# Kernel tuning notes

Measured on AMD Instinct MI355X. Metric: run time of the kernel, lower is better.

## Reference

```python
import jax, jax.numpy as jnp
import numpy as np

B, S, D = 64, 512, 1024   # batch, max_phon_seq_len, d_model
V = 64                    # phonological vocabulary size
T = 131072                # total ragged tokens (avg 4 per (batch, position) slot)


def setup_inputs() -> dict:
    key = jax.random.key(0)
    k1, k2, k3, k4 = jax.random.split(key, 4)
    tokens = jax.random.randint(k1, (T,), 0, V)                      # flat token indices
    segment_ids = jnp.sort(jax.random.randint(k2, (T,), 0, B * S))   # sorted segment id per token
    phon_embedding = jax.random.normal(k3, (V, D), dtype=jnp.float32)
    phon_pos_embedding = jax.random.normal(k4, (S, D), dtype=jnp.float32)
    return {
        "tokens": tokens,
        "segment_ids": segment_ids,
        "phon_embedding": phon_embedding,
        "phon_pos_embedding": phon_pos_embedding,
    }


def reference(tokens, segment_ids, phon_embedding, phon_pos_embedding):
    # Fused ragged segment-mean embedding (EmbeddingBag 'mean' semantics):
    # for each (batch, position) segment, mean of embeddings of its tokens.
    gathered = phon_embedding[tokens]                                   # [T, D]
    sums = jax.ops.segment_sum(gathered, segment_ids, num_segments=B * S)          # [B*S, D]
    counts = jax.ops.segment_sum(jnp.ones((T,), dtype=gathered.dtype),
                                 segment_ids, num_segments=B * S)       # [B*S]
    means = sums / jnp.maximum(counts, 1.0)[:, None]                    # empty slots stay zero
    # add positional embedding, as in embed_phon_tokens
    out = means.reshape(B, S, D) + phon_pos_embedding[None, :, :]       # [B, S, D]
    return out
```

## Files before the change

### kernel.cpp

```cpp
#include <hip/hip_runtime.h>
#include <hip/hip_bf16.h>

#define BB 64
#define SS 512
#define DD 1024
#define NSEG (BB * SS)

typedef float floatx4 __attribute__((ext_vector_type(4)));

__global__ __launch_bounds__(256) void fill_bounds_kernel(
    const int* __restrict__ seg_ids,
    int* __restrict__ seg_start,
    int T)
{
    int t = blockIdx.x * blockDim.x + threadIdx.x;
    if (t >= T) return;
    int cur  = seg_ids[t];
    int prev = (t == 0) ? -1 : seg_ids[t - 1];
    for (int s = prev + 1; s <= cur; ++s) seg_start[s] = t;
    if (t == T - 1) {
        for (int s = cur + 1; s <= NSEG; ++s) seg_start[s] = T;
    }
}

__global__ __launch_bounds__(256) void seg_mean_embed_kernel(
    const int* __restrict__ tokens,
    const int* __restrict__ seg_start,
    const float* __restrict__ emb,
    const float* __restrict__ pos,
    float* __restrict__ out)
{
    const int seg = blockIdx.x;
    const int lo = seg_start[seg];
    const int hi = seg_start[seg + 1];

    const int d = threadIdx.x * 4;

    floatx4 acc = (floatx4)(0.f);
    for (int t = lo; t < hi; ++t) {
        const int tok = tokens[t];
        const floatx4 v = *reinterpret_cast<const floatx4*>(emb + (size_t)tok * DD + d);
        acc += v;
    }

    const int cnt = hi - lo;
    const float inv = (cnt > 0) ? (1.0f / (float)cnt) : 0.0f;

    const int s = seg & (SS - 1);
    const floatx4 p = *reinterpret_cast<const floatx4*>(pos + (size_t)s * DD + d);

    floatx4 o = acc * inv + p;

    *reinterpret_cast<floatx4*>(out + (size_t)seg * DD + d) = o;
}

__device__ __forceinline__ int lower_bound_dev(const int* __restrict__ a, int n, int key) {
    int lo = 0, hi = n;
    while (lo < hi) {
        int mid = (lo + hi) >> 1;
        if (a[mid] < key) lo = mid + 1; else hi = mid;
    }
    return lo;
}

__global__ __launch_bounds__(256) void seg_mean_embed_bsearch_kernel(
    const int* __restrict__ tokens,
    const int* __restrict__ seg_ids,
    const float* __restrict__ emb,
    const float* __restrict__ pos,
    float* __restrict__ out,
    int T)
{
    const int seg = blockIdx.x;
    const int lo = lower_bound_dev(seg_ids, T, seg);
    const int hi = lower_bound_dev(seg_ids, T, seg + 1);
    const int d = threadIdx.x * 4;

    floatx4 acc = (floatx4)(0.f);
    for (int t = lo; t < hi; ++t) {
        const int tok = tokens[t];
        const floatx4 v = *reinterpret_cast<const floatx4*>(emb + (size_t)tok * DD + d);
        acc += v;
    }
    const int cnt = hi - lo;
    const float inv = (cnt > 0) ? (1.0f / (float)cnt) : 0.0f;
    const int s = seg & (SS - 1);
    const floatx4 p = *reinterpret_cast<const floatx4*>(pos + (size_t)s * DD + d);
    floatx4 o = acc * inv + p;
    *reinterpret_cast<floatx4*>(out + (size_t)seg * DD + d) = o;
}

extern "C" void kernel_launch(void* const* d_in, const int* in_sizes, int n_in,
                              void* d_out, int out_size, void* d_ws, size_t ws_size,
                              hipStream_t stream) {
    const int*   tokens  = (const int*)d_in[0];
    const int*   seg_ids = (const int*)d_in[1];
    const float* emb     = (const float*)d_in[2];
    const float* pos     = (const float*)d_in[3];
    float*       out     = (float*)d_out;
    const int T = in_sizes[0];

    const size_t need = (size_t)(NSEG + 1) * sizeof(int);
    if (ws_size >= need) {
        int* seg_start = (int*)d_ws;
        fill_bounds_kernel<<<(T + 255) / 256, 256, 0, stream>>>(seg_ids, seg_start, T);
        seg_mean_embed_kernel<<<NSEG, 256, 0, stream>>>(tokens, seg_start, emb, pos, out);
    } else {
        seg_mean_embed_bsearch_kernel<<<NSEG, 256, 0, stream>>>(tokens, seg_ids, emb, pos, out, T);
    }
}
```

Measured before the change: 43.14 us.

## Stage embedding table halves in LDS as bf16 and batch segments per block

Replaces the one-block-per-segment kernel with blocks that each copy half of the 64x1024 embedding table into shared memory, converted to bf16. Each block then processes 128 segments, one wave per segment at a time, with 8 columns per lane. The aim is to cut repeated global/L2 gathers of embedding rows and the per-block launch overhead. In exchange, every block redundantly loads and converts 128KB of the table, and the 64KB of LDS per block limits occupancy. Storing the table in bf16 also adds rounding error to the means, which is a precision trade-off.

```diff
diff --git a/kernel.cpp b/kernel.cpp
--- a/kernel.cpp
+++ b/kernel.cpp
@@ -4,9 +4,25 @@
 #define BB 64
 #define SS 512
 #define DD 1024
+#define VV 64
 #define NSEG (BB * SS)
+#define HALF 512
+#define SEGS_PER_BLK 128
+#define THREADS 512
 
 typedef float floatx4 __attribute__((ext_vector_type(4)));
+
+__device__ __forceinline__ ushort f32_to_bf16_rne(float f) {
+    unsigned int b = __float_as_uint(f);
+    unsigned int r = b + 0x7fffu + ((b >> 16) & 1u);
+    return (ushort)(r >> 16);
+}
+__device__ __forceinline__ float bf16lo_to_f32(unsigned int u) {
+    return __uint_as_float(u << 16);
+}
+__device__ __forceinline__ float bf16hi_to_f32(unsigned int u) {
+    return __uint_as_float(u & 0xffff0000u);
+}
 
 __global__ __launch_bounds__(256) void fill_bounds_kernel(
     const int* __restrict__ seg_ids,
@@ -23,35 +39,74 @@
     }
 }
 
-__global__ __launch_bounds__(256) void seg_mean_embed_kernel(
+__global__ __launch_bounds__(THREADS, 4) void seg_mean_lds_kernel(
     const int* __restrict__ tokens,
     const int* __restrict__ seg_start,
     const float* __restrict__ emb,
     const float* __restrict__ pos,
     float* __restrict__ out)
 {
-    const int seg = blockIdx.x;
-    const int lo = seg_start[seg];
-    const int hi = seg_start[seg + 1];
+    __shared__ ushort s_emb[VV * HALF];
 
-    const int d = threadIdx.x * 4;
+    const int bid     = blockIdx.x;
+    const int half    = bid & 1;
+    const int segbase = (bid >> 1) * SEGS_PER_BLK;
+    const int tid     = threadIdx.x;
 
-    floatx4 acc = (floatx4)(0.f);
-    for (int t = lo; t < hi; ++t) {
-        const int tok = tokens[t];
-        const floatx4 v = *reinterpret_cast<const floatx4*>(emb + (size_t)tok * DD + d);
-        acc += v;
+    const float* src = emb + half * HALF;
+    #pragma unroll
+    for (int k = 0; k < (VV * HALF) / (THREADS * 4); ++k) {
+        const int flat = k * THREADS * 4 + tid * 4;
+        const int row  = flat >> 9;
+        const int col  = flat & (HALF - 1);
+        const floatx4 v = *reinterpret_cast<const floatx4*>(src + (size_t)row * DD + col);
+        ushort4 u;
+        u.x = f32_to_bf16_rne(v.x);
+        u.y = f32_to_bf16_rne(v.y);
+        u.z = f32_to_bf16_rne(v.z);
+        u.w = f32_to_bf16_rne(v.w);
+        *reinterpret_cast<ushort4*>(&s_emb[flat]) = u;
     }
+    __syncthreads();
 
-    const int cnt = hi - lo;
-    const float inv = (cnt > 0) ? (1.0f / (float)cnt) : 0.0f;
+    const int wave    = tid >> 6;
+    const int lane    = tid & 63;
+    const int colbase = lane * 8;
 
-    const int s = seg & (SS - 1);
-    const floatx4 p = *reinterpret_cast<const floatx4*>(pos + (size_t)s * DD + d);
+    #pragma unroll 1
+    for (int i = 0; i < SEGS_PER_BLK / 8; ++i) {
+        const int seg = segbase + i * 8 + wave;
+        const int lo  = seg_start[seg];
+        const int hi  = seg_start[seg + 1];
 
-    floatx4 o = acc * inv + p;
+        float acc[8] = {0.f, 0.f, 0.f, 0.f, 0.f, 0.f, 0.f, 0.f};
+        for (int t = lo; t < hi; ++t) {
+            const int tok = tokens[t];
+            const uint4 u = *reinterpret_cast<const uint4*>(&s_emb[tok * HALF + colbase]);
+            acc[0] += bf16lo_to_f32(u.x); acc[1] += bf16hi_to_f32(u.x);
+            acc[2] += bf16lo_to_f32(u.y); acc[3] += bf16hi_to_f32(u.y);
+            acc[4] += bf16lo_to_f32(u.z); acc[5] += bf16hi_to_f32(u.z);
+            acc[6] += bf16lo_to_f32(u.w); acc[7] += bf16hi_to_f32(u.w);
+        }
 
-    *reinterpret_cast<floatx4*>(out + (size_t)seg * DD + d) = o;
+        const int cnt = hi - lo;
+        const float inv = (cnt > 0) ? (1.0f / (float)cnt) : 0.0f;
+
+        const int s = seg & (SS - 1);
+        const float* pp = pos + (size_t)s * DD + half * HALF + colbase;
+        const floatx4 p0 = *reinterpret_cast<const floatx4*>(pp);
+        const floatx4 p1 = *reinterpret_cast<const floatx4*>(pp + 4);
+
+        floatx4 o0, o1;
+        o0.x = acc[0] * inv + p0.x;  o0.y = acc[1] * inv + p0.y;
+        o0.z = acc[2] * inv + p0.z;  o0.w = acc[3] * inv + p0.w;
+        o1.x = acc[4] * inv + p1.x;  o1.y = acc[5] * inv + p1.y;
+        o1.z = acc[6] * inv + p1.z;  o1.w = acc[7] * inv + p1.w;
+
+        float* op = out + (size_t)seg * DD + half * HALF + colbase;
+        *reinterpret_cast<floatx4*>(op)     = o0;
+        *reinterpret_cast<floatx4*>(op + 4) = o1;
+    }
 }
 
 __device__ __forceinline__ int lower_bound_dev(const int* __restrict__ a, int n, int key) {
@@ -104,7 +159,8 @@
     if (ws_size >= need) {
         int* seg_start = (int*)d_ws;
         fill_bounds_kernel<<<(T + 255) / 256, 256, 0, stream>>>(seg_ids, seg_start, T);
-        seg_mean_embed_kernel<<<NSEG, 256, 0, stream>>>(tokens, seg_start, emb, pos, out);
+        const int grid = (NSEG / SEGS_PER_BLK) * 2;
+        seg_mean_lds_kernel<<<grid, THREADS, 0, stream>>>(tokens, seg_start, emb, pos, out);
     } else {
         seg_mean_embed_bsearch_kernel<<<NSEG, 256, 0, stream>>>(tokens, seg_ids, emb, pos, out, T);
     }
```

After: 50.93 us. 1.18x slower.

## Group eight segments per block, stage tokens in LDS, gather bf16 table

Applied to the files above, without the earlier changes.

Converts the fp32 embedding table to a bf16 copy in workspace with a small pre-kernel. The main kernel processes eight segments per block, staging their token indices in shared memory, then accumulates bf16 rows in fp32. Output is written with nontemporal stores. The aim is to cut block launch overhead and gather traffic and to avoid polluting the cache with output. In exchange it adds a kernel launch and reduces embedding precision.

```diff
diff --git a/kernel.cpp b/kernel.cpp
--- a/kernel.cpp
+++ b/kernel.cpp
@@ -4,9 +4,24 @@
 #define BB 64
 #define SS 512
 #define DD 1024
+#define VV 64
 #define NSEG (BB * SS)
+#define G_SEGS 8
+#define CAP 2048
 
 typedef float floatx4 __attribute__((ext_vector_type(4)));
+
+__device__ __forceinline__ ushort f32_to_bf16_rne(float f) {
+    unsigned int b = __float_as_uint(f);
+    unsigned int r = b + 0x7fffu + ((b >> 16) & 1u);
+    return (ushort)(r >> 16);
+}
+__device__ __forceinline__ float bf16lo_to_f32(unsigned int u) {
+    return __uint_as_float(u << 16);
+}
+__device__ __forceinline__ float bf16hi_to_f32(unsigned int u) {
+    return __uint_as_float(u & 0xffff0000u);
+}
 
 __global__ __launch_bounds__(256) void fill_bounds_kernel(
     const int* __restrict__ seg_ids,
@@ -23,35 +38,74 @@
     }
 }
 
-__global__ __launch_bounds__(256) void seg_mean_embed_kernel(
+__global__ __launch_bounds__(256) void conv_emb_kernel(
+    const float* __restrict__ emb,
+    ushort* __restrict__ tbl)
+{
+    const int i = (blockIdx.x * 256 + threadIdx.x) * 4;
+    const floatx4 v = *reinterpret_cast<const floatx4*>(emb + i);
+    ushort4 u;
+    u.x = f32_to_bf16_rne(v.x);
+    u.y = f32_to_bf16_rne(v.y);
+    u.z = f32_to_bf16_rne(v.z);
+    u.w = f32_to_bf16_rne(v.w);
+    *reinterpret_cast<ushort4*>(tbl + i) = u;
+}
+
+__global__ __launch_bounds__(256) void seg_mean_g8_kernel(
     const int* __restrict__ tokens,
     const int* __restrict__ seg_start,
-    const float* __restrict__ emb,
+    const ushort* __restrict__ tbl,
     const float* __restrict__ pos,
     float* __restrict__ out)
 {
-    const int seg = blockIdx.x;
-    const int lo = seg_start[seg];
-    const int hi = seg_start[seg + 1];
+    __shared__ int s_bnd[G_SEGS + 1];
+    __shared__ int s_tok[CAP];
 
-    const int d = threadIdx.x * 4;
+    const int g0  = blockIdx.x * G_SEGS;
+    const int tid = threadIdx.x;
 
-    floatx4 acc = (floatx4)(0.f);
-    for (int t = lo; t < hi; ++t) {
-        const int tok = tokens[t];
-        const floatx4 v = *reinterpret_cast<const floatx4*>(emb + (size_t)tok * DD + d);
-        acc += v;
+    if (tid <= G_SEGS) s_bnd[tid] = seg_start[g0 + tid];
+    __syncthreads();
+
+    const int lo0   = s_bnd[0];
+    const int total = s_bnd[G_SEGS] - lo0;
+    const int n_lds = (total < CAP) ? total : CAP;
+    for (int j = tid; j < n_lds; j += 256) s_tok[j] = tokens[lo0 + j];
+    __syncthreads();
+
+    const int d = tid * 4;
+
+    #pragma unroll 1
+    for (int s = 0; s < G_SEGS; ++s) {
+        const int seg = g0 + s;
+        const int lo  = s_bnd[s];
+        const int hi  = s_bnd[s + 1];
+
+        float a0 = 0.f, a1 = 0.f, a2 = 0.f, a3 = 0.f;
+        for (int t = lo; t < hi; ++t) {
+            const int idx = t - lo0;
+            const int tok = (idx < CAP) ? s_tok[idx] : tokens[t];
+            const uint2 u = *reinterpret_cast<const uint2*>(tbl + tok * DD + d);
+            a0 += bf16lo_to_f32(u.x); a1 += bf16hi_to_f32(u.x);
+            a2 += bf16lo_to_f32(u.y); a3 += bf16hi_to_f32(u.y);
+        }
+
+        const int cnt = hi - lo;
+        const float inv = (cnt > 0) ? (1.0f / (float)cnt) : 0.0f;
+
+        const floatx4 p = *reinterpret_cast<const floatx4*>(
+            pos + (size_t)(seg & (SS - 1)) * DD + d);
+
+        floatx4 o;
+        o.x = a0 * inv + p.x;
+        o.y = a1 * inv + p.y;
+        o.z = a2 * inv + p.z;
+        o.w = a3 * inv + p.w;
+
+        __builtin_nontemporal_store(o, reinterpret_cast<floatx4*>(
+            out + (size_t)seg * DD + d));
     }
-
-    const int cnt = hi - lo;
-    const float inv = (cnt > 0) ? (1.0f / (float)cnt) : 0.0f;
-
-    const int s = seg & (SS - 1);
-    const floatx4 p = *reinterpret_cast<const floatx4*>(pos + (size_t)s * DD + d);
-
-    floatx4 o = acc * inv + p;
-
-    *reinterpret_cast<floatx4*>(out + (size_t)seg * DD + d) = o;
 }
 
 __device__ __forceinline__ int lower_bound_dev(const int* __restrict__ a, int n, int key) {
@@ -100,11 +154,14 @@
     float*       out     = (float*)d_out;
     const int T = in_sizes[0];
 
-    const size_t need = (size_t)(NSEG + 1) * sizeof(int);
+    const size_t tbl_bytes = (size_t)VV * DD * sizeof(ushort);
+    const size_t need = tbl_bytes + (size_t)(NSEG + 1) * sizeof(int);
     if (ws_size >= need) {
-        int* seg_start = (int*)d_ws;
+        ushort* tbl       = (ushort*)d_ws;
+        int*    seg_start = (int*)((char*)d_ws + tbl_bytes);
         fill_bounds_kernel<<<(T + 255) / 256, 256, 0, stream>>>(seg_ids, seg_start, T);
-        seg_mean_embed_kernel<<<NSEG, 256, 0, stream>>>(tokens, seg_start, emb, pos, out);
+        conv_emb_kernel<<<(VV * DD) / (256 * 4), 256, 0, stream>>>(emb, tbl);
+        seg_mean_g8_kernel<<<NSEG / G_SEGS, 256, 0, stream>>>(tokens, seg_start, tbl, pos, out);
     } else {
         seg_mean_embed_bsearch_kernel<<<NSEG, 256, 0, stream>>>(tokens, seg_ids, emb, pos, out, T);
     }
```

Result: slower. 47.03 us (+9.0%).

## Recast segment-mean embedding as token-count histogram times bf16 embedding GEMM

Applied to the files above, without the earlier changes.

Builds a per-segment token histogram over the 64-word vocabulary, swizzles the embedding table into bf16 MFMA operand layout, and computes segment sums as a matrix multiply with MFMA instructions, fusing the mean scaling and positional add into the epilogue with nontemporal stores. This replaces per-token gathers of embedding rows with dense matrix math. In exchange it adds two extra kernel launches, a histogram buffer round-trip through memory, and reduces embedding precision to bf16.

```diff
diff --git a/kernel.cpp b/kernel.cpp
--- a/kernel.cpp
+++ b/kernel.cpp
@@ -4,9 +4,17 @@
 #define BB 64
 #define SS 512
 #define DD 1024
+#define VV 64
 #define NSEG (BB * SS)
 
-typedef float floatx4 __attribute__((ext_vector_type(4)));
+typedef float f32x4 __attribute__((ext_vector_type(4)));
+typedef short bf16x8 __attribute__((ext_vector_type(8)));
+
+__device__ __forceinline__ ushort f32_to_bf16_rne(float f) {
+    unsigned int b = __float_as_uint(f);
+    unsigned int r = b + 0x7fffu + ((b >> 16) & 1u);
+    return (ushort)(r >> 16);
+}
 
 __global__ __launch_bounds__(256) void fill_bounds_kernel(
     const int* __restrict__ seg_ids,
@@ -23,35 +31,129 @@
     }
 }
 
-__global__ __launch_bounds__(256) void seg_mean_embed_kernel(
+__global__ __launch_bounds__(256) void build_h_kernel(
     const int* __restrict__ tokens,
     const int* __restrict__ seg_start,
+    float* __restrict__ H)
+{
+    __shared__ float h[256 * VV];
+    const int tid  = threadIdx.x;
+    const int seg0 = blockIdx.x * 256;
+    for (int i = tid; i < 256 * VV; i += 256) h[i] = 0.f;
+    __syncthreads();
+    const int seg = seg0 + tid;
+    const int lo = seg_start[seg];
+    const int hi = seg_start[seg + 1];
+    for (int t = lo; t < hi; ++t) h[tid * VV + tokens[t]] += 1.f;
+    __syncthreads();
+    const f32x4* src = (const f32x4*)h;
+    f32x4* dst = (f32x4*)(H + (size_t)seg0 * VV);
+    for (int i = tid; i < 256 * VV / 4; i += 256) dst[i] = src[i];
+}
+
+__global__ __launch_bounds__(256) void swz_emb_kernel(
     const float* __restrict__ emb,
+    ushort* __restrict__ A)
+{
+    const int g    = blockIdx.x * 256 + threadIdx.x;
+    const int lane = g & 63;
+    const int tile = g >> 6;
+    const int ks   = tile & 1;
+    const int mt   = tile >> 1;
+    const int dim  = mt * 16 + (lane & 15);
+    const int v0   = ks * 32 + (lane >> 4) * 8;
+    bf16x8 w;
+    #pragma unroll
+    for (int j = 0; j < 8; ++j)
+        w[j] = (short)f32_to_bf16_rne(emb[(size_t)(v0 + j) * DD + dim]);
+    *reinterpret_cast<bf16x8*>(A + (size_t)g * 8) = w;
+}
+
+#define MW 64
+#define NW 32
+__global__ __launch_bounds__(256) void gemm_kernel(
+    const ushort* __restrict__ A,
+    const float* __restrict__ H,
+    const int* __restrict__ seg_start,
     const float* __restrict__ pos,
     float* __restrict__ out)
 {
-    const int seg = blockIdx.x;
-    const int lo = seg_start[seg];
-    const int hi = seg_start[seg + 1];
-
-    const int d = threadIdx.x * 4;
-
-    floatx4 acc = (floatx4)(0.f);
-    for (int t = lo; t < hi; ++t) {
-        const int tok = tokens[t];
-        const floatx4 v = *reinterpret_cast<const floatx4*>(emb + (size_t)tok * DD + d);
-        acc += v;
-    }
-
-    const int cnt = hi - lo;
-    const float inv = (cnt > 0) ? (1.0f / (float)cnt) : 0.0f;
-
-    const int s = seg & (SS - 1);
-    const floatx4 p = *reinterpret_cast<const floatx4*>(pos + (size_t)s * DD + d);
-
-    floatx4 o = acc * inv + p;
-
-    *reinterpret_cast<floatx4*>(out + (size_t)seg * DD + d) = o;
+    const int warp = threadIdx.x >> 6;
+    const int lane = threadIdx.x & 63;
+    const int mgrp = blockIdx.x & 15;
+    const int ngrp = blockIdx.x >> 4;
+    const int m_base = mgrp * MW;
+    const int n_base = ngrp * (NW * 4) + warp * NW;
+
+    const int mt0 = m_base >> 4;
+    bf16x8 a[4][2];
+    #pragma unroll
+    for (int mi = 0; mi < 4; ++mi)
+        #pragma unroll
+        for (int ks = 0; ks < 2; ++ks)
+            a[mi][ks] = *reinterpret_cast<const bf16x8*>(
+                A + ((size_t)((mt0 + mi) * 2 + ks) * 64 + lane) * 8);
+
+    bf16x8 b[2][2];
+    #pragma unroll
+    for (int ni = 0; ni < 2; ++ni) {
+        const int seg = n_base + ni * 16 + (lane & 15);
+        const float* hrow = H + (size_t)seg * VV + (lane >> 4) * 8;
+        #pragma unroll
+        for (int ks = 0; ks < 2; ++ks) {
+            const f32x4 h0 = *reinterpret_cast<const f32x4*>(hrow + ks * 32);
+            const f32x4 h1 = *reinterpret_cast<const f32x4*>(hrow + ks * 32 + 4);
+            bf16x8 w;
+            w[0] = (short)(__float_as_uint(h0[0]) >> 16);
+            w[1] = (short)(__float_as_uint(h0[1]) >> 16);
+            w[2] = (short)(__float_as_uint(h0[2]) >> 16);
+            w[3] = (short)(__float_as_uint(h0[3]) >> 16);
+            w[4] = (short)(__float_as_uint(h1[0]) >> 16);
+            w[5] = (short)(__float_as_uint(h1[1]) >> 16);
+            w[6] = (short)(__float_as_uint(h1[2]) >> 16);
+            w[7] = (short)(__float_as_uint(h1[3]) >> 16);
+            b[ni][ks] = w;
+        }
+    }
+
+    f32x4 acc[4][2];
+    #pragma unroll
+    for (int mi = 0; mi < 4; ++mi)
+        #pragma unroll
+        for (int ni = 0; ni < 2; ++ni)
+            acc[mi][ni] = (f32x4)(0.f);
+
+    #pragma unroll
+    for (int ks = 0; ks < 2; ++ks)
+        #pragma unroll
+        for (int mi = 0; mi < 4; ++mi)
+            #pragma unroll
+            for (int ni = 0; ni < 2; ++ni)
+                acc[mi][ni] = __builtin_amdgcn_mfma_f32_16x16x32_bf16(
+                    a[mi][ks], b[ni][ks], acc[mi][ni], 0, 0, 0);
+
+    float inv[2];
+    #pragma unroll
+    for (int ni = 0; ni < 2; ++ni) {
+        const int seg = n_base + ni * 16 + (lane & 15);
+        const int cnt = seg_start[seg + 1] - seg_start[seg];
+        inv[ni] = (cnt > 0) ? (1.0f / (float)cnt) : 0.0f;
+    }
+    const int dimq = (lane >> 4) * 4;
+    #pragma unroll
+    for (int ni = 0; ni < 2; ++ni) {
+        const int seg  = n_base + ni * 16 + (lane & 15);
+        const int srow = seg & (SS - 1);
+        #pragma unroll
+        for (int mi = 0; mi < 4; ++mi) {
+            const int dim = m_base + mi * 16 + dimq;
+            const f32x4 p = *reinterpret_cast<const f32x4*>(
+                pos + (size_t)srow * DD + dim);
+            f32x4 o = acc[mi][ni] * inv[ni] + p;
+            __builtin_nontemporal_store(o,
+                reinterpret_cast<f32x4*>(out + (size_t)seg * DD + dim));
+        }
+    }
 }
 
 __device__ __forceinline__ int lower_bound_dev(const int* __restrict__ a, int n, int key) {
@@ -76,18 +178,17 @@
     const int hi = lower_bound_dev(seg_ids, T, seg + 1);
     const int d = threadIdx.x * 4;
 
-    floatx4 acc = (floatx4)(0.f);
+    f32x4 acc = (f32x4)(0.f);
     for (int t = lo; t < hi; ++t) {
         const int tok = tokens[t];
-        const floatx4 v = *reinterpret_cast<const floatx4*>(emb + (size_t)tok * DD + d);
-        acc += v;
+        acc += *reinterpret_cast<const f32x4*>(emb + (size_t)tok * DD + d);
     }
     const int cnt = hi - lo;
     const float inv = (cnt > 0) ? (1.0f / (float)cnt) : 0.0f;
     const int s = seg & (SS - 1);
-    const floatx4 p = *reinterpret_cast<const floatx4*>(pos + (size_t)s * DD + d);
-    floatx4 o = acc * inv + p;
-    *reinterpret_cast<floatx4*>(out + (size_t)seg * DD + d) = o;
+    const f32x4 p = *reinterpret_cast<const f32x4*>(pos + (size_t)s * DD + d);
+    f32x4 o = acc * inv + p;
+    *reinterpret_cast<f32x4*>(out + (size_t)seg * DD + d) = o;
 }
 
 extern "C" void kernel_launch(void* const* d_in, const int* in_sizes, int n_in,
@@ -100,11 +201,19 @@
     float*       out     = (float*)d_out;
     const int T = in_sizes[0];
 
-    const size_t need = (size_t)(NSEG + 1) * sizeof(int);
+    const size_t a_bytes  = (size_t)128 * 64 * 8 * sizeof(ushort);
+    const size_t h_bytes  = (size_t)NSEG * VV * sizeof(float);
+    const size_t need = a_bytes + h_bytes + (size_t)(NSEG + 1) * sizeof(int);
+
     if (ws_size >= need) {
-        int* seg_start = (int*)d_ws;
+        ushort* A         = (ushort*)d_ws;
+        float*  H         = (float*)((char*)d_ws + a_bytes);
+        int*    seg_start = (int*)((char*)d_ws + a_bytes + h_bytes);
+
         fill_bounds_kernel<<<(T + 255) / 256, 256, 0, stream>>>(seg_ids, seg_start, T);
-        seg_mean_embed_kernel<<<NSEG, 256, 0, stream>>>(tokens, seg_start, emb, pos, out);
+        build_h_kernel<<<NSEG / 256, 256, 0, stream>>>(tokens, seg_start, H);
+        swz_emb_kernel<<<32, 256, 0, stream>>>(emb, A);
+        gemm_kernel<<<4096, 256, 0, stream>>>(A, H, seg_start, pos, out);
     } else {
         seg_mean_embed_bsearch_kernel<<<NSEG, 256, 0, stream>>>(tokens, seg_ids, emb, pos, out, T);
     }
```

After: 67.78 us. +57.1%, slower.
